# Performance work log

Hardware: AMD Instinct MI355X
Metric: run time of the kernel (lower is better)

## Reference

```python
import jax, jax.numpy as jnp
import numpy as np
import math

B, T, C, H = 4, 2048, 1024, 16

def setup_inputs() -> dict:
    key = jax.random.key(0)
    ks = jax.random.split(key, 7)
    s = 0.02
    return {
        'x':  jax.random.normal(ks[0], (B, T, C), dtype=jnp.float32),
        'Wq': jax.random.normal(ks[1], (C, C), dtype=jnp.float32) * s,
        'bq': jnp.zeros((C,), dtype=jnp.float32),
        'Wk': jax.random.normal(ks[2], (C, C), dtype=jnp.float32) * s,
        'bk': jnp.zeros((C,), dtype=jnp.float32),
        'Wv': jax.random.normal(ks[3], (C, C), dtype=jnp.float32) * s,
        'bv': jnp.zeros((C,), dtype=jnp.float32),
    }

def reference(x, Wq, bq, Wk, bk, Wv, bv):
    # Dropouts are identity (eval mode). Note: the original module reuses
    # v_proj as the output projection -- reproduced faithfully.
    b, t, c = x.shape
    hs = c // H
    q = (x @ Wq + bq).reshape(b, t, H, hs).transpose(0, 2, 1, 3)  # [B,H,T,hs]
    k = (x @ Wk + bk).reshape(b, t, H, hs).transpose(0, 2, 1, 3)
    v = (x @ Wv + bv).reshape(b, t, H, hs).transpose(0, 2, 1, 3)
    att = jnp.einsum('bhqd,bhkd->bhqk', q, k) * (1.0 / math.sqrt(hs))
    causal = jnp.tril(jnp.ones((t, t), dtype=bool))
    att = jnp.where(causal[None, None], att, -jnp.inf)
    att = jax.nn.softmax(att, axis=-1)
    y = jnp.einsum('bhqk,bhkd->bhqd', att, v)  # [B,H,T,hs]
    y = y.transpose(0, 2, 1, 3).reshape(b, t, c)
    y = y @ Wv + bv  # module applies v_proj again as output projection
    return y
```

## Files before the change

kernel.cpp:

```cpp
#include <hip/hip_runtime.h>
#include <hip/hip_bf16.h>

typedef __bf16 bf16;
typedef __attribute__((ext_vector_type(8))) __bf16 bf16x8;
typedef __attribute__((ext_vector_type(4))) __bf16 bf16x4;
typedef __attribute__((ext_vector_type(2))) __bf16 bf16x2;
typedef __attribute__((ext_vector_type(4))) float f32x4;
typedef __attribute__((ext_vector_type(2))) unsigned int u32x2;
typedef __attribute__((ext_vector_type(4))) unsigned int u32x4;

#define MFMA16(a, b, c) __builtin_amdgcn_mfma_f32_16x16x32_bf16((a), (b), (c), 0, 0, 0)
#define SM_SCALE 0.18033688011112043f

__device__ __forceinline__ void gld_lds16(const bf16* g, bf16* l) {
    __builtin_amdgcn_global_load_lds((const __attribute__((address_space(1))) void*)g,
                                     (__attribute__((address_space(3))) void*)l, 16, 0, 0);
}

#define PBAR() asm volatile("s_barrier" ::: "memory")
#define VWAIT0() asm volatile("s_waitcnt vmcnt(0)" ::: "memory")

__global__ __launch_bounds__(256) void cvt_x(const float* __restrict__ in,
                                             bf16* __restrict__ outb, int n) {
    int i = (blockIdx.x * 256 + threadIdx.x) * 4;
    if (i + 3 < n) {
        const float4 v = *(const float4*)(in + i);
        bf16x4 o = {(bf16)v.x, (bf16)v.y, (bf16)v.z, (bf16)v.w};
        *(bf16x4*)(outb + i) = o;
    }
}

__global__ __launch_bounds__(256) void transpose_w3(const float* __restrict__ W0,
                                                    const float* __restrict__ W1,
                                                    const float* __restrict__ W2,
                                                    bf16* __restrict__ Wt) {
    const float* W = (blockIdx.z == 0) ? W0 : ((blockIdx.z == 1) ? W1 : W2);
    bf16* dst = Wt + (size_t)blockIdx.z * 1024 * 1024;
    __shared__ float tile[64][65];
    const int r0 = blockIdx.y * 64;
    const int c0 = blockIdx.x * 64;
    const int tid = threadIdx.x;
    for (int i = tid; i < 4096; i += 256) {
        int r = i >> 6, cc = i & 63;
        tile[r][cc] = W[(size_t)(r0 + r) * 1024 + c0 + cc];
    }
    __syncthreads();
    for (int i = tid; i < 4096; i += 256) {
        int n = i >> 6, k = i & 63;
        dst[(size_t)(c0 + n) * 1024 + r0 + k] = (bf16)tile[k][n];
    }
}

#define QKV_PHASE(MH, COFF, READB)                                                        \
    {                                                                                     \
        if (READB) {                                                                      \
            _Pragma("unroll") for (int ni = 0; ni < 4; ni++) bfrag[ni] =                  \
                *(const bf16x8*)&Bsp[((wc * 64 + ni * 16 + l16) << 6) + (COFF)];          \
        }                                                                                 \
        bf16x8 af[4];                                                                     \
        _Pragma("unroll") for (int m4 = 0; m4 < 4; m4++) af[m4] =                         \
            *(const bf16x8*)&Asp[((wr * 128 + (MH)*64 + m4 * 16 + l16) << 6) + (COFF)];   \
        __builtin_amdgcn_s_setprio(1);                                                    \
        _Pragma("unroll") for (int m4 = 0; m4 < 4; m4++)                                  \
            _Pragma("unroll") for (int ni = 0; ni < 4; ni++) acc[(MH)*4 + m4][ni] =       \
                MFMA16(af[m4], bfrag[ni], acc[(MH)*4 + m4][ni]);                          \
        __builtin_amdgcn_s_setprio(0);                                                    \
    }

__global__ __launch_bounds__(512, 2) void gemm_qkv(const bf16* __restrict__ A,
                                                   const bf16* __restrict__ Bt,
                                                   const float* __restrict__ b0,
                                                   const float* __restrict__ b1,
                                                   const float* __restrict__ b2,
                                                   bf16* __restrict__ qb,
                                                   bf16* __restrict__ kb,
                                                   bf16* __restrict__ Vt) {
    __shared__ alignas(16) bf16 LDS[65536];

    const int orig = blockIdx.x;
    const int swz = (orig & 7) * 48 + (orig >> 3);
    const int by = swz / 12, bx = swz % 12;
    const int m0 = by * 256, n0 = bx * 256;

    const int tid = threadIdx.x;
    const int wid = tid >> 6, lane = tid & 63;
    const int wr = wid >> 2, wc = wid & 3;
    const int quad = lane >> 4, l16 = lane & 15;

    const int sr = tid >> 3;
    const int scol = ((tid & 7) * 8) ^ ((sr & 7) * 8);
    const bf16* gA = A + (size_t)(m0 + sr) * 1024 + scol;
    const bf16* gB = Bt + (size_t)(n0 + sr) * 1024 + scol;
    bf16* lbase = &LDS[tid * 8];

    const int xorE = (l16 & 7) * 8;
    const int coff0 = (quad * 8) ^ xorE;
    const int coff1 = (32 + quad * 8) ^ xorE;

    f32x4 acc[8][4] = {};
    bf16x8 bfrag[4];

    auto STAGE = [&](int kt, int p) {
        const bf16* a = gA + kt * 64;
        const bf16* b = gB + kt * 64;
        bf16* la = lbase + p * 32768;
        bf16* lb = la + 16384;
        gld_lds16(a, la);
        gld_lds16(a + 64 * 1024, la + 4096);
        gld_lds16(a + 128 * 1024, la + 8192);
        gld_lds16(a + 192 * 1024, la + 12288);
        gld_lds16(b, lb);
        gld_lds16(b + 64 * 1024, lb + 4096);
        gld_lds16(b + 128 * 1024, lb + 8192);
        gld_lds16(b + 192 * 1024, lb + 12288);
    };

    STAGE(0, 0);
    VWAIT0();
    PBAR();

#pragma unroll 1
    for (int kt = 0; kt < 16; kt++) {
        const int p = kt & 1;
        const bf16* Asp = &LDS[p * 32768];
        const bf16* Bsp = Asp + 16384;
        if (kt + 1 < 16) STAGE(kt + 1, p ^ 1);
        QKV_PHASE(0, coff0, true);
        PBAR();
        QKV_PHASE(1, coff0, false);
        PBAR();
        QKV_PHASE(0, coff1, true);
        PBAR();
        QKV_PHASE(1, coff1, false);
        if (kt + 1 < 16) {
            VWAIT0();
            PBAR();
        }
    }

    const int sel = n0 >> 10;
    const int nl0 = (n0 & 1023) + wc * 64;
    const int mb0 = m0 + wr * 128;
    if (sel < 2) {
        const float* bias = (sel == 0) ? b0 : b1;
        bf16* Cp = (sel == 0) ? qb : kb;
        const float qs = (sel == 0) ? SM_SCALE : 1.0f;
#pragma unroll
        for (int mi = 0; mi < 8; mi++) {
            const int mbase = mb0 + mi * 16 + quad * 4;
#pragma unroll
            for (int ni = 0; ni < 4; ni++) {
                const int nl = nl0 + ni * 16 + l16;
                const float bv = bias[nl];
#pragma unroll
                for (int r = 0; r < 4; r++)
                    Cp[(size_t)(mbase + r) * 1024 + nl] = (bf16)((acc[mi][ni][r] + bv) * qs);
            }
        }
    } else {
        const int b = m0 >> 11;
#pragma unroll
        for (int ni = 0; ni < 4; ni++) {
            const int nl = nl0 + ni * 16 + l16;
            const int h = nl >> 6, d = nl & 63;
            const float bv = b2[nl];
            bf16* dst = Vt + ((size_t)(b * 16 + h) * 64 + d) * 2048;
#pragma unroll
            for (int mi = 0; mi < 8; mi++) {
                const int t0 = (mb0 + mi * 16 + quad * 4) & 2047;
                bf16x4 w = {(bf16)(acc[mi][ni][0] + bv), (bf16)(acc[mi][ni][1] + bv),
                            (bf16)(acc[mi][ni][2] + bv), (bf16)(acc[mi][ni][3] + bv)};
                *(bf16x4*)&dst[t0] = w;
            }
        }
    }
}

template <int MODE>
__global__ __launch_bounds__(256) void gemm_bt(const bf16* __restrict__ A,
                                               const bf16* __restrict__ Bt,
                                               const float* __restrict__ b0,
                                               void* __restrict__ out0,
                                               int M, int N, int K) {
    __shared__ alignas(16) bf16 As[128 * 32];
    __shared__ alignas(16) bf16 Bs[128 * 32];
    const int tid = threadIdx.x;
    const int wave = tid >> 6, lane = tid & 63;
    const int quad = lane >> 4, l16 = lane & 15;
    const int m0 = blockIdx.y * 128, n0 = blockIdx.x * 128;
    const int wm = (wave & 1) * 64, wn = (wave >> 1) * 64;

    f32x4 acc[4][4] = {};

    const int srow = lane >> 2, scol = (lane & 3) * 8;
    const bf16* ga = A + (size_t)(m0 + wave * 32 + srow) * K + scol;
    const bf16* gb = Bt + (size_t)(n0 + wave * 32 + srow) * K + scol;
    bf16* la = &As[(wave * 32) * 32];
    bf16* lb = &Bs[(wave * 32) * 32];

    for (int k0 = 0; k0 < K; k0 += 32) {
        __syncthreads();
        gld_lds16(ga + k0, la);
        gld_lds16(ga + k0 + (size_t)16 * K, la + 16 * 32);
        gld_lds16(gb + k0, lb);
        gld_lds16(gb + k0 + (size_t)16 * K, lb + 16 * 32);
        __syncthreads();
        bf16x8 af[4], bfr[4];
#pragma unroll
        for (int mi = 0; mi < 4; mi++)
            af[mi] = *(const bf16x8*)&As[(wm + mi * 16 + l16) * 32 + quad * 8];
#pragma unroll
        for (int ni = 0; ni < 4; ni++)
            bfr[ni] = *(const bf16x8*)&Bs[(wn + ni * 16 + l16) * 32 + quad * 8];
#pragma unroll
        for (int mi = 0; mi < 4; mi++)
#pragma unroll
            for (int ni = 0; ni < 4; ni++)
                acc[mi][ni] = MFMA16(af[mi], bfr[ni], acc[mi][ni]);
    }

    float* Cp = (float*)out0;
#pragma unroll
    for (int mi = 0; mi < 4; mi++) {
        const int mbase = m0 + wm + mi * 16 + quad * 4;
#pragma unroll
        for (int ni = 0; ni < 4; ni++) {
            const int n = n0 + wn + ni * 16 + l16;
            const float bv = b0[n];
#pragma unroll
            for (int r = 0; r < 4; r++)
                Cp[(size_t)(mbase + r) * 1024 + n] = acc[mi][ni][r] + bv;
        }
    }
}

template <bool NEEDMASK>
__device__ __forceinline__ void softmax_reg(const f32x4* st, float& l_i, bf16x8* pf,
                                            int qrel) {
    unsigned int p[4][2];
#pragma unroll
    for (int j = 0; j < 4; j++) {
        float pv[4];
#pragma unroll
        for (int r = 0; r < 4; r++) {
            float s = st[j][r];
            if (NEEDMASK && (j * 16 + r > qrel)) s = -1e30f;
            const float e = exp2f(s);
            l_i += e;
            pv[r] = e;
        }
        bf16x2 w0 = {(bf16)pv[0], (bf16)pv[1]};
        bf16x2 w1 = {(bf16)pv[2], (bf16)pv[3]};
        p[j][0] = __builtin_bit_cast(unsigned int, w0);
        p[j][1] = __builtin_bit_cast(unsigned int, w1);
    }
#pragma unroll
    for (int ks = 0; ks < 2; ks++) {
        unsigned int q4[4];
#pragma unroll
        for (int h = 0; h < 2; h++) {
            u32x2 s32 = __builtin_amdgcn_permlane32_swap(p[2 * ks][h], p[2 * ks + 1][h],
                                                         false, false);
            u32x2 s16 = __builtin_amdgcn_permlane16_swap(s32[0], s32[1], false, false);
            q4[h] = s16[0];
            q4[2 + h] = s16[1];
        }
        u32x4 qq = {q4[0], q4[1], q4[2], q4[3]};
        pf[ks] = __builtin_bit_cast(bf16x8, qq);
    }
}

__global__ __launch_bounds__(256, 4) void attn(const bf16* __restrict__ Q,
                                               const bf16* __restrict__ Kg,
                                               const bf16* __restrict__ Vt,
                                               bf16* __restrict__ O) {
    const int lin = blockIdx.y * 16 + blockIdx.x;
    const int bh = (lin & 7) * 8 + ((lin >> 3) & 7);
    const int jb = lin >> 6;
    const int b = bh >> 4, h = bh & 15;
    const int tid = threadIdx.x;
    const int wave = tid >> 6, lane = tid & 63;
    const int quad = lane >> 4, l16 = lane & 15;

    __shared__ alignas(16) bf16 KVs[2 * 128 * 72];

    const bf16* Kbase = Kg + ((size_t)b * 2048) * 1024 + h * 64;
    const bf16* Vbase = Vt + (size_t)bh * 64 * 2048;

    const int ra = tid >> 3, oa = (tid & 7) * 8;

#pragma unroll 1
    for (int phase = 0; phase < 2; phase++) {
        const int qs = (phase == 0) ? (31 - jb) : jb;
        const int q0 = qs * 64;
        const bf16* Qbase = Q + ((size_t)(b * 2048 + q0)) * 1024 + h * 64;

        bf16x8 qf[2];
#pragma unroll
        for (int ks = 0; ks < 2; ks++)
            qf[ks] = *(const bf16x8*)&Qbase[(size_t)(wave * 16 + l16) * 1024 + ks * 32 + quad * 8];

        float l_i = 0.f;
        f32x4 ot[4] = {};
        const int ntiles = qs + 1;
        const int qrel = wave * 16 + l16 - quad * 4;

        const bf16* pK0 = Kbase + (size_t)ra * 1024 + oa;
        const bf16* pK1 = Kbase + (size_t)(ra + 32) * 1024 + oa;
        const bf16* pV0 = Vbase + (size_t)ra * 2048 + oa;
        const bf16* pV1 = Vbase + (size_t)(ra + 32) * 2048 + oa;

        bf16x8 rc0 = *(const bf16x8*)pK0, rc1 = *(const bf16x8*)pK1;
        bf16x8 rc2 = *(const bf16x8*)pV0, rc3 = *(const bf16x8*)pV1;
        bf16x8 rn0, rn1, rn2, rn3;

#pragma unroll 1
        for (int tk = 0; tk < ntiles; tk++) {
            if (tk + 1 < ntiles) {
                rn0 = *(const bf16x8*)(pK0 + 64 * 1024);
                rn1 = *(const bf16x8*)(pK1 + 64 * 1024);
                rn2 = *(const bf16x8*)(pV0 + 64);
                rn3 = *(const bf16x8*)(pV1 + 64);
                pK0 += 64 * 1024; pK1 += 64 * 1024; pV0 += 64; pV1 += 64;
            }
            bf16* buf = &KVs[(tk & 1) * (128 * 72)];
            *(bf16x8*)&buf[ra * 72 + oa] = rc0;
            *(bf16x8*)&buf[(ra + 32) * 72 + oa] = rc1;
            *(bf16x8*)&buf[(64 + ra) * 72 + oa] = rc2;
            *(bf16x8*)&buf[(64 + ra + 32) * 72 + oa] = rc3;
            __syncthreads();

            f32x4 st[4] = {};
#pragma unroll
            for (int ks = 0; ks < 2; ks++)
#pragma unroll
                for (int j = 0; j < 4; j++) {
                    const bf16x8 kf =
                        *(const bf16x8*)&buf[(j * 16 + l16) * 72 + ks * 32 + quad * 8];
                    st[j] = MFMA16(kf, qf[ks], st[j]);
                }

            bf16x8 pf[2];
            if (tk == ntiles - 1)
                softmax_reg<true>(st, l_i, pf, qrel);
            else
                softmax_reg<false>(st, l_i, pf, qrel);

#pragma unroll
            for (int ks = 0; ks < 2; ks++)
#pragma unroll
                for (int db = 0; db < 4; db++) {
                    const bf16x8 vf =
                        *(const bf16x8*)&buf[(64 + db * 16 + l16) * 72 + ks * 32 + quad * 8];
                    ot[db] = MFMA16(vf, pf[ks], ot[db]);
                }
            rc0 = rn0; rc1 = rn1; rc2 = rn2; rc3 = rn3;
        }

        l_i += __shfl_xor(l_i, 16, 64);
        l_i += __shfl_xor(l_i, 32, 64);

        bf16* ep = &KVs[(ntiles & 1) * (128 * 72) + (wave * 16) * 72];
        const float inv = 1.f / l_i;
#pragma unroll
        for (int db = 0; db < 4; db++) {
            bf16x4 w = {(bf16)(ot[db][0] * inv), (bf16)(ot[db][1] * inv),
                        (bf16)(ot[db][2] * inv), (bf16)(ot[db][3] * inv)};
            *(bf16x4*)&ep[l16 * 72 + db * 16 + quad * 4] = w;
        }
        {
            const int orow = lane >> 2, oc = (lane & 3) * 16;
            bf16* Obase =
                O + ((size_t)(b * 2048 + q0 + wave * 16 + orow)) * 1024 + h * 64 + oc;
            const bf16* src = &ep[orow * 72 + oc];
            *(bf16x8*)&Obase[0] = *(const bf16x8*)&src[0];
            *(bf16x8*)&Obase[8] = *(const bf16x8*)&src[8];
        }
        __syncthreads();
    }
}

extern "C" void kernel_launch(void* const* d_in, const int* in_sizes, int n_in,
                              void* d_out, int out_size, void* d_ws, size_t ws_size,
                              hipStream_t stream) {
    const float* x = (const float*)d_in[0];
    const float* Wq = (const float*)d_in[1];
    const float* bq = (const float*)d_in[2];
    const float* Wk = (const float*)d_in[3];
    const float* bk = (const float*)d_in[4];
    const float* Wv = (const float*)d_in[5];
    const float* bv = (const float*)d_in[6];
    float* out = (float*)d_out;

    const int M = 8192;
    const size_t sz_x = (size_t)M * 1024;
    const size_t sz_w = (size_t)1024 * 1024;

    char* p = (char*)d_ws;
    bf16* xb = (bf16*)p;   p += sz_x * 2;
    bf16* Wcat = (bf16*)p; p += 3 * sz_w * 2;
    bf16* qb = (bf16*)p;   p += sz_x * 2;
    bf16* kb = (bf16*)p;   p += sz_x * 2;
    bf16* Vt = (bf16*)p;   p += sz_x * 2;
    bf16* yatt = (bf16*)p; p += sz_x * 2;

    cvt_x<<<dim3(8192), dim3(256), 0, stream>>>(x, xb, (int)sz_x);
    transpose_w3<<<dim3(16, 16, 3), dim3(256), 0, stream>>>(Wq, Wk, Wv, Wcat);

    gemm_qkv<<<dim3(384), dim3(512), 0, stream>>>(xb, Wcat, bq, bk, bv, qb, kb, Vt);
    attn<<<dim3(16, 64), dim3(256), 0, stream>>>(qb, kb, Vt, yatt);
    gemm_bt<1><<<dim3(8, 64), dim3(256), 0, stream>>>(yatt, Wcat + 2 * sz_w, bv,
                                                      out, M, 1024, 1024);
}
```

Before: 268.6 us.

## Fuse x conversion into QKV GEMM and use direct-to-LDS loads in attention

Removes the separate fp32-to-bf16 conversion kernel. The QKV GEMM now loads fp32 x into registers, converts it, and writes it to swizzled LDS, while B keeps its async global-to-LDS path. The attention kernel replaces register-staged K/V tiles with global_load_lds into XOR-swizzled unpadded LDS, and computes the softmax row sum with an MFMA against a ones vector instead of scalar adds and shuffles. The GEMM now reads A at twice the bytes per tile from fp32 and holds more registers. The extra MFMAs per tile add matrix-core work in exchange for fewer VALU and shuffle operations.

```diff
diff --git a/kernel.cpp b/kernel.cpp
--- a/kernel.cpp
+++ b/kernel.cpp
@@ -19,16 +19,7 @@
 
 #define PBAR() asm volatile("s_barrier" ::: "memory")
 #define VWAIT0() asm volatile("s_waitcnt vmcnt(0)" ::: "memory")
-
-__global__ __launch_bounds__(256) void cvt_x(const float* __restrict__ in,
-                                             bf16* __restrict__ outb, int n) {
-    int i = (blockIdx.x * 256 + threadIdx.x) * 4;
-    if (i + 3 < n) {
-        const float4 v = *(const float4*)(in + i);
-        bf16x4 o = {(bf16)v.x, (bf16)v.y, (bf16)v.z, (bf16)v.w};
-        *(bf16x4*)(outb + i) = o;
-    }
-}
+#define LWAIT0() asm volatile("s_waitcnt lgkmcnt(0)" ::: "memory")
 
 __global__ __launch_bounds__(256) void transpose_w3(const float* __restrict__ W0,
                                                     const float* __restrict__ W1,
@@ -67,7 +58,7 @@
         __builtin_amdgcn_s_setprio(0);                                                    \
     }
 
-__global__ __launch_bounds__(512, 2) void gemm_qkv(const bf16* __restrict__ A,
+__global__ __launch_bounds__(512, 2) void gemm_qkv(const float* __restrict__ Af,
                                                    const bf16* __restrict__ Bt,
                                                    const float* __restrict__ b0,
                                                    const float* __restrict__ b1,
@@ -88,8 +79,8 @@
     const int quad = lane >> 4, l16 = lane & 15;
 
     const int sr = tid >> 3;
-    const int scol = ((tid & 7) * 8) ^ ((sr & 7) * 8);
-    const bf16* gA = A + (size_t)(m0 + sr) * 1024 + scol;
+    const int scol = (((tid & 7) ^ (sr & 7)) * 8);
+    const float* gA = Af + (size_t)(m0 + sr) * 1024 + scol;
     const bf16* gB = Bt + (size_t)(n0 + sr) * 1024 + scol;
     bf16* lbase = &LDS[tid * 8];
 
@@ -99,24 +90,41 @@
 
     f32x4 acc[8][4] = {};
     bf16x8 bfrag[4];
-
-    auto STAGE = [&](int kt, int p) {
-        const bf16* a = gA + kt * 64;
+    float4 av[8];
+
+    auto LOADA = [&](int kt) {
+        const float* a = gA + kt * 64;
+#pragma unroll
+        for (int i = 0; i < 4; i++) {
+            av[2 * i] = *(const float4*)(a + (size_t)i * 64 * 1024);
+            av[2 * i + 1] = *(const float4*)(a + (size_t)i * 64 * 1024 + 4);
+        }
+    };
+    auto WRITEA = [&](int p) {
+        bf16* la = lbase + p * 32768;
+#pragma unroll
+        for (int i = 0; i < 4; i++) {
+            bf16x8 w = {(bf16)av[2 * i].x,     (bf16)av[2 * i].y,
+                        (bf16)av[2 * i].z,     (bf16)av[2 * i].w,
+                        (bf16)av[2 * i + 1].x, (bf16)av[2 * i + 1].y,
+                        (bf16)av[2 * i + 1].z, (bf16)av[2 * i + 1].w};
+            *(bf16x8*)&la[i * 4096] = w;
+        }
+    };
+    auto STAGEB = [&](int kt, int p) {
         const bf16* b = gB + kt * 64;
-        bf16* la = lbase + p * 32768;
-        bf16* lb = la + 16384;
-        gld_lds16(a, la);
-        gld_lds16(a + 64 * 1024, la + 4096);
-        gld_lds16(a + 128 * 1024, la + 8192);
-        gld_lds16(a + 192 * 1024, la + 12288);
+        bf16* lb = lbase + p * 32768 + 16384;
         gld_lds16(b, lb);
         gld_lds16(b + 64 * 1024, lb + 4096);
         gld_lds16(b + 128 * 1024, lb + 8192);
         gld_lds16(b + 192 * 1024, lb + 12288);
     };
 
-    STAGE(0, 0);
+    LOADA(0);
+    STAGEB(0, 0);
     VWAIT0();
+    WRITEA(0);
+    LWAIT0();
     PBAR();
 
 #pragma unroll 1
@@ -124,16 +132,23 @@
         const int p = kt & 1;
         const bf16* Asp = &LDS[p * 32768];
         const bf16* Bsp = Asp + 16384;
-        if (kt + 1 < 16) STAGE(kt + 1, p ^ 1);
+        if (kt + 1 < 16) {
+            LOADA(kt + 1);
+            STAGEB(kt + 1, p ^ 1);
+        }
         QKV_PHASE(0, coff0, true);
         PBAR();
         QKV_PHASE(1, coff0, false);
         PBAR();
         QKV_PHASE(0, coff1, true);
+        if (kt + 1 < 16) {
+            VWAIT0();
+            WRITEA(p ^ 1);
+        }
         PBAR();
         QKV_PHASE(1, coff1, false);
         if (kt + 1 < 16) {
-            VWAIT0();
+            LWAIT0();
             PBAR();
         }
     }
@@ -235,8 +250,7 @@
 }
 
 template <bool NEEDMASK>
-__device__ __forceinline__ void softmax_reg(const f32x4* st, float& l_i, bf16x8* pf,
-                                            int qrel) {
+__device__ __forceinline__ void softmax_reg(const f32x4* st, bf16x8* pf, int qrel) {
     unsigned int p[4][2];
 #pragma unroll
     for (int j = 0; j < 4; j++) {
@@ -245,9 +259,7 @@
         for (int r = 0; r < 4; r++) {
             float s = st[j][r];
             if (NEEDMASK && (j * 16 + r > qrel)) s = -1e30f;
-            const float e = exp2f(s);
-            l_i += e;
-            pv[r] = e;
+            pv[r] = exp2f(s);
         }
         bf16x2 w0 = {(bf16)pv[0], (bf16)pv[1]};
         bf16x2 w1 = {(bf16)pv[2], (bf16)pv[3]};
@@ -282,12 +294,20 @@
     const int wave = tid >> 6, lane = tid & 63;
     const int quad = lane >> 4, l16 = lane & 15;
 
-    __shared__ alignas(16) bf16 KVs[2 * 128 * 72];
+    __shared__ alignas(16) bf16 KVs[2 * 8192];
 
     const bf16* Kbase = Kg + ((size_t)b * 2048) * 1024 + h * 64;
     const bf16* Vbase = Vt + (size_t)bh * 64 * 2048;
 
-    const int ra = tid >> 3, oa = (tid & 7) * 8;
+    const int srow = tid >> 3;
+    const int schunk = (tid & 7) ^ (srow & 7);
+
+    const int xorE = (l16 & 7) * 8;
+    const int cofA = (quad * 8) ^ xorE;
+    const int cofB = (32 + quad * 8) ^ xorE;
+
+    const bf16 one1 = (bf16)1.0f;
+    const bf16x8 onesf = {one1, one1, one1, one1, one1, one1, one1, one1};
 
 #pragma unroll 1
     for (int phase = 0; phase < 2; phase++) {
@@ -300,35 +320,38 @@
         for (int ks = 0; ks < 2; ks++)
             qf[ks] = *(const bf16x8*)&Qbase[(size_t)(wave * 16 + l16) * 1024 + ks * 32 + quad * 8];
 
-        float l_i = 0.f;
         f32x4 ot[4] = {};
+        f32x4 lacc = {0.f, 0.f, 0.f, 0.f};
         const int ntiles = qs + 1;
         const int qrel = wave * 16 + l16 - quad * 4;
 
-        const bf16* pK0 = Kbase + (size_t)ra * 1024 + oa;
-        const bf16* pK1 = Kbase + (size_t)(ra + 32) * 1024 + oa;
-        const bf16* pV0 = Vbase + (size_t)ra * 2048 + oa;
-        const bf16* pV1 = Vbase + (size_t)(ra + 32) * 2048 + oa;
-
-        bf16x8 rc0 = *(const bf16x8*)pK0, rc1 = *(const bf16x8*)pK1;
-        bf16x8 rc2 = *(const bf16x8*)pV0, rc3 = *(const bf16x8*)pV1;
-        bf16x8 rn0, rn1, rn2, rn3;
+        const bf16* pK = Kbase + (size_t)srow * 1024 + schunk * 8;
+        const bf16* pK2 = pK + (size_t)32 * 1024;
+        const bf16* pV = Vbase + (size_t)srow * 2048 + schunk * 8;
+        const bf16* pV2 = pV + (size_t)32 * 2048;
+
+        {
+            bf16* nb = &KVs[tid * 8];
+            gld_lds16(pK, nb);
+            gld_lds16(pK2, nb + 2048);
+            gld_lds16(pV, nb + 4096);
+            gld_lds16(pV2, nb + 6144);
+            pK += 64 * 1024; pK2 += 64 * 1024; pV += 64; pV2 += 64;
+        }
+        VWAIT0();
+        PBAR();
 
 #pragma unroll 1
         for (int tk = 0; tk < ntiles; tk++) {
+            const bf16* buf = &KVs[(tk & 1) * 8192];
             if (tk + 1 < ntiles) {
-                rn0 = *(const bf16x8*)(pK0 + 64 * 1024);
-                rn1 = *(const bf16x8*)(pK1 + 64 * 1024);
-                rn2 = *(const bf16x8*)(pV0 + 64);
-                rn3 = *(const bf16x8*)(pV1 + 64);
-                pK0 += 64 * 1024; pK1 += 64 * 1024; pV0 += 64; pV1 += 64;
+                bf16* nb = &KVs[((tk + 1) & 1) * 8192 + tid * 8];
+                gld_lds16(pK, nb);
+                gld_lds16(pK2, nb + 2048);
+                gld_lds16(pV, nb + 4096);
+                gld_lds16(pV2, nb + 6144);
+                pK += 64 * 1024; pK2 += 64 * 1024; pV += 64; pV2 += 64;
             }
-            bf16* buf = &KVs[(tk & 1) * (128 * 72)];
-            *(bf16x8*)&buf[ra * 72 + oa] = rc0;
-            *(bf16x8*)&buf[(ra + 32) * 72 + oa] = rc1;
-            *(bf16x8*)&buf[(64 + ra) * 72 + oa] = rc2;
-            *(bf16x8*)&buf[(64 + ra + 32) * 72 + oa] = rc3;
-            __syncthreads();
 
             f32x4 st[4] = {};
 #pragma unroll
@@ -336,32 +359,34 @@
 #pragma unroll
                 for (int j = 0; j < 4; j++) {
                     const bf16x8 kf =
-                        *(const bf16x8*)&buf[(j * 16 + l16) * 72 + ks * 32 + quad * 8];
+                        *(const bf16x8*)&buf[(j * 16 + l16) * 64 + (ks ? cofB : cofA)];
                     st[j] = MFMA16(kf, qf[ks], st[j]);
                 }
 
             bf16x8 pf[2];
             if (tk == ntiles - 1)
-                softmax_reg<true>(st, l_i, pf, qrel);
+                softmax_reg<true>(st, pf, qrel);
             else
-                softmax_reg<false>(st, l_i, pf, qrel);
+                softmax_reg<false>(st, pf, qrel);
+
+            lacc = MFMA16(onesf, pf[0], lacc);
+            lacc = MFMA16(onesf, pf[1], lacc);
 
 #pragma unroll
             for (int ks = 0; ks < 2; ks++)
 #pragma unroll
                 for (int db = 0; db < 4; db++) {
-                    const bf16x8 vf =
-                        *(const bf16x8*)&buf[(64 + db * 16 + l16) * 72 + ks * 32 + quad * 8];
+                    const bf16x8 vf = *(const bf16x8*)&buf[4096 + (db * 16 + l16) * 64 +
+                                                           (ks ? cofB : cofA)];
                     ot[db] = MFMA16(vf, pf[ks], ot[db]);
                 }
-            rc0 = rn0; rc1 = rn1; rc2 = rn2; rc3 = rn3;
-        }
-
-        l_i += __shfl_xor(l_i, 16, 64);
-        l_i += __shfl_xor(l_i, 32, 64);
-
-        bf16* ep = &KVs[(ntiles & 1) * (128 * 72) + (wave * 16) * 72];
-        const float inv = 1.f / l_i;
+
+            if (tk + 1 < ntiles) VWAIT0();
+            PBAR();
+        }
+
+        const float inv = 1.f / lacc[0];
+        bf16* ep = &KVs[(ntiles & 1) * 8192 + wave * (16 * 72)];
 #pragma unroll
         for (int db = 0; db < 4; db++) {
             bf16x4 w = {(bf16)(ot[db][0] * inv), (bf16)(ot[db][1] * inv),
@@ -397,17 +422,15 @@
     const size_t sz_w = (size_t)1024 * 1024;
 
     char* p = (char*)d_ws;
-    bf16* xb = (bf16*)p;   p += sz_x * 2;
     bf16* Wcat = (bf16*)p; p += 3 * sz_w * 2;
     bf16* qb = (bf16*)p;   p += sz_x * 2;
     bf16* kb = (bf16*)p;   p += sz_x * 2;
     bf16* Vt = (bf16*)p;   p += sz_x * 2;
     bf16* yatt = (bf16*)p; p += sz_x * 2;
 
-    cvt_x<<<dim3(8192), dim3(256), 0, stream>>>(x, xb, (int)sz_x);
     transpose_w3<<<dim3(16, 16, 3), dim3(256), 0, stream>>>(Wq, Wk, Wv, Wcat);
 
-    gemm_qkv<<<dim3(384), dim3(512), 0, stream>>>(xb, Wcat, bq, bk, bv, qb, kb, Vt);
+    gemm_qkv<<<dim3(384), dim3(512), 0, stream>>>(x, Wcat, bq, bk, bv, qb, kb, Vt);
     attn<<<dim3(16, 64), dim3(256), 0, stream>>>(qb, kb, Vt, yatt);
     gemm_bt<1><<<dim3(8, 64), dim3(256), 0, stream>>>(yatt, Wcat + 2 * sz_w, bv,
                                                       out, M, 1024, 1024);
```

Result: slower. 277.1 us (+3.1%).
